# Performance work log

Hardware: AMD Instinct MI355X
Metric: run time of the kernel (lower is better)

The kernel has to match this reference:

```python
import jax, jax.numpy as jnp
import numpy as np

H = 256      # input_size == hidden_size
N = 512      # x dim0: acts as LSTM time axis (torch unbatched 2D LSTM input)
S = 128      # x dim1: independent seq positions (outer python loop in torch)
UP = 4       # upscale


def setup_inputs() -> dict:
    key = jax.random.key(0)
    ks = jax.random.split(key, 9)
    k_init = 1.0 / np.sqrt(H)
    u = lambda k, shape: jax.random.uniform(k, shape, jnp.float32, -k_init, k_init)
    return {
        "x": jax.random.normal(ks[0], (N, S, H), jnp.float32),
        # PyTorch nn.LSTM params, gate order (i, f, g, o)
        "Wih0": u(ks[1], (4 * H, H)), "Whh0": u(ks[2], (4 * H, H)),
        "bih0": u(ks[3], (4 * H,)),   "bhh0": u(ks[4], (4 * H,)),
        "Wih1": u(ks[5], (4 * H, H)), "Whh1": u(ks[6], (4 * H, H)),
        "bih1": u(ks[7], (4 * H,)),   "bhh1": u(ks[8], (4 * H,)),
    }


def _lstm_layer(x, h0, c0, Wih, Whh, b):
    """Scan one LSTM layer over the time axis. x: [N, S, H], h0/c0: [S, H]."""
    def step(carry, xt):
        h, c = carry
        g = xt @ Wih.T + h @ Whh.T + b            # [S, 4H]
        i, f, gg, o = jnp.split(g, 4, axis=-1)
        i = jax.nn.sigmoid(i)
        f = jax.nn.sigmoid(f)
        gg = jnp.tanh(gg)
        o = jax.nn.sigmoid(o)
        c = f * c + i * gg
        h = o * jnp.tanh(c)
        return (h, c), h
    (hT, cT), ys = jax.lax.scan(step, (h0, c0), x)
    return ys, hT, cT


def reference(x, Wih0, Whh0, bih0, bhh0, Wih1, Whh1, bih1, bhh1):
    n, s, hdim = x.shape
    # state per seq position (torch's outer loop is vectorized as batch S)
    h = jnp.zeros((2, s, hdim), x.dtype)
    c = jnp.zeros((2, s, hdim), x.dtype)
    b0 = bih0 + bhh0
    b1 = bih1 + bhh1
    data = [x]
    cur = x
    for _ in range(UP - 1):
        y0, h0n, c0n = _lstm_layer(cur, h[0], c[0], Wih0, Whh0, b0)
        y1, h1n, c1n = _lstm_layer(y0, h[1], c[1], Wih1, Whh1, b1)
        h = jnp.stack([h0n, h1n])
        c = jnp.stack([c0n, c1n])
        cur = y1
        data.append(y1)
    # torch interleaves per seq position: [..., s*UP + k, ...] = data[k][:, s, :]
    out = jnp.stack(data, axis=2)          # [N, S, UP, H]
    return out.reshape(n, s * UP, hdim)
```

## Files before the change

kernel.cpp:

```cpp
#include <hip/hip_runtime.h>
#include <stdint.h>

#define Hh 256
#define Sd 128
#define Nt 512
#define NPASS 3
#define TSTEPS (NPASS*Nt)
#define RBLK 16
#define POIS 0x7F80u
#define LEAD 192

typedef float f32x4 __attribute__((ext_vector_type(4)));
typedef __bf16 bf16x8 __attribute__((ext_vector_type(8)));
typedef unsigned short u16x8 __attribute__((ext_vector_type(8)));
typedef unsigned long long ull;
typedef ull ull2 __attribute__((ext_vector_type(2)));

#define HBUF_ELEMS ((size_t)Nt*Sd*Hh)
#define WPACK_OFF  (2ull*HBUF_ELEMS*2)
#define FLAGS_OFF  (WPACK_OFF + 2097152ull)

__device__ __forceinline__ unsigned short f2bf(float f) {
  unsigned u = __builtin_bit_cast(unsigned, f);
  u += 0x7FFFu + ((u >> 16) & 1u);
  return (unsigned short)(u >> 16);
}
__device__ __forceinline__ ull pk4(float a, float b, float c, float d) {
  return (ull)f2bf(a) | ((ull)f2bf(b) << 16) | ((ull)f2bf(c) << 32) | ((ull)f2bf(d) << 48);
}
__device__ __forceinline__ bool hasPois(ull v) {
  return ((unsigned short)(v)       == (unsigned short)POIS) |
         ((unsigned short)(v >> 16) == (unsigned short)POIS) |
         ((unsigned short)(v >> 32) == (unsigned short)POIS) |
         ((unsigned short)(v >> 48) == (unsigned short)POIS);
}
__device__ __forceinline__ ull ld8(const void* p) {
  return __hip_atomic_load((ull*)p, __ATOMIC_RELAXED, __HIP_MEMORY_SCOPE_AGENT);
}
__device__ __forceinline__ void st8c(void* p, ull v) {
  __hip_atomic_store((ull*)p, v, __ATOMIC_RELAXED, __HIP_MEMORY_SCOPE_AGENT);
}

__global__ void pack_w(const float* __restrict__ Wih0, const float* __restrict__ Whh0,
                       const float* __restrict__ Wih1, const float* __restrict__ Whh1,
                       unsigned short* __restrict__ wpack) {
  int id = blockIdx.x * 256 + threadIdx.x;
  int ln = id & 63;
  int kt = (id >> 6) & 15;
  int w  = (id >> 10) & 7;
  int g2 = (id >> 13) & 7;
  int l  = (id >> 16) & 1;
  int col = (w >> 1)*256 + g2*32 + (w & 1)*16 + (ln & 15);
  int k0 = kt*32 + (ln >> 4)*8;
  const float* Wih = l ? Wih1 : Wih0;
  const float* Whh = l ? Whh1 : Whh0;
  const float* src = (k0 < 256) ? (Wih + (size_t)col*256 + k0)
                                : (Whh + (size_t)col*256 + (k0 - 256));
  u16x8 v;
#pragma unroll
  for (int j = 0; j < 8; ++j) v[j] = f2bf(src[j]);
  *(u16x8*)(wpack + (size_t)id * 8) = v;
}

__global__ void copy_x(const float* __restrict__ x, float* __restrict__ out) {
  int id = blockIdx.x * 256 + threadIdx.x;
  int n  = id >> 13;
  int s  = (id >> 6) & 127;
  int h4 = id & 63;
  const float4 v = *(const float4*)(x + ((size_t)n*Sd + s)*Hh + h4*4);
  *(float4*)(out + ((size_t)n*(Sd*4) + s*4)*Hh + h4*4) = v;
}

__global__ void poison_hbuf(unsigned int* __restrict__ p) {
  size_t i = (size_t)blockIdx.x * 256 + threadIdx.x;
  uint4 v = make_uint4(0x7F807F80u, 0x7F807F80u, 0x7F807F80u, 0x7F807F80u);
  *(uint4*)(p + i*4) = v;
}

__global__ void __launch_bounds__(512) lstm_persist(
    const float* __restrict__ x,
    const float* __restrict__ bih0, const float* __restrict__ bhh0,
    const float* __restrict__ bih1, const float* __restrict__ bhh1,
    const unsigned short* __restrict__ wpack,
    unsigned short* __restrict__ hbuf,
    unsigned int* __restrict__ prog,
    float* __restrict__ out)
{
  const int b = blockIdx.x;
  const int r = b & 7;
  const int g2 = (b >> 3) & 7;
  const int l = (b >> 6) & 1;
  const int tid = threadIdx.x;
  const int ln = tid & 63;
  const int w  = tid >> 6;

  __shared__ __align__(16) unsigned short Ain[RBLK * 256];
  __shared__ __align__(16) unsigned short Ah [RBLK * 256];
  __shared__ float gates[RBLK][132];

  bf16x8 B[16];
  {
    const unsigned short* base = wpack + ((size_t)((l*8 + g2)*8 + w)) * 8192 + (size_t)ln * 8;
#pragma unroll
    for (int kt = 0; kt < 16; ++kt) {
      u16x8 u = *(const u16x8*)(base + kt * 512);
      B[kt] = __builtin_bit_cast(bf16x8, u);
    }
  }

  const int srow = tid >> 5;
  const int cc   = tid & 31;
  const int s    = r*RBLK + srow;
  const int hcol = g2*32 + cc;
  float bias[4];
  {
    const float* bi = l ? bih1 : bih0;
    const float* bh = l ? bhh1 : bhh0;
#pragma unroll
    for (int q = 0; q < 4; ++q) {
      int col = q*256 + g2*32 + cc;
      bias[q] = bi[col] + bh[col];
    }
  }
  float cst = 0.f;

  const int row_f = ln & 15;
  const int kg16  = (ln >> 4) * 16;
  const int swr   = (row_f & 7) << 4;
  const int stAddr = srow*512 + ((cc*16) ^ ((srow & 7) << 4));

  unsigned int* flagL1 = prog + r*8;
  unsigned int* myFlag = prog + r*8 + g2;
  const unsigned short* hbufL0 = hbuf;
  unsigned short* hbufSelf = hbuf + (size_t)l * HBUF_ELEMS;

  auto stageAin = [&](int T1) {
    const int t1 = T1 & 511, p1 = T1 >> 9;
    if (l == 1) {
      const ull* ip = (const ull*)(hbufL0 + ((size_t)t1*Sd + s)*Hh + cc*8);
      ull a0 = ld8(ip), a1 = ld8(ip + 1);
      while (hasPois(a0)) { __builtin_amdgcn_s_sleep(1); a0 = ld8(ip); }
      while (hasPois(a1)) { __builtin_amdgcn_s_sleep(1); a1 = ld8(ip + 1); }
      ull2 v = {a0, a1}; *(ull2*)((char*)Ain + stAddr) = v;
    } else if (p1 == 0) {
      const float* xb = x + ((size_t)t1*Sd + s)*Hh + cc*8;
      float4 v0 = *(const float4*)(xb);
      float4 v1 = *(const float4*)(xb + 4);
      ull2 v = {pk4(v0.x, v0.y, v0.z, v0.w), pk4(v1.x, v1.y, v1.z, v1.w)};
      *(ull2*)((char*)Ain + stAddr) = v;
    } else {
      const ull* op = (const ull*)(out + ((size_t)t1*(Sd*4) + s*4 + p1)*Hh + cc*8);
      ull o0 = ld8(op), o1 = ld8(op+1), o2 = ld8(op+2), o3 = ld8(op+3);
      float f0 = __builtin_bit_cast(float, (unsigned)(o0 & 0xFFFFFFFFu));
      float f1 = __builtin_bit_cast(float, (unsigned)(o0 >> 32));
      float f2 = __builtin_bit_cast(float, (unsigned)(o1 & 0xFFFFFFFFu));
      float f3 = __builtin_bit_cast(float, (unsigned)(o1 >> 32));
      float f4 = __builtin_bit_cast(float, (unsigned)(o2 & 0xFFFFFFFFu));
      float f5 = __builtin_bit_cast(float, (unsigned)(o2 >> 32));
      float f6 = __builtin_bit_cast(float, (unsigned)(o3 & 0xFFFFFFFFu));
      float f7 = __builtin_bit_cast(float, (unsigned)(o3 >> 32));
      ull2 v = {pk4(f0, f1, f2, f3), pk4(f4, f5, f6, f7)};
      *(ull2*)((char*)Ain + stAddr) = v;
    }
  };

#define MFMA4(BUF, BOFF)                                                            \
  {                                                                                 \
    _Pragma("unroll")                                                               \
    for (int kt = 0; kt < 8; kt += 2) {                                             \
      int off0 = row_f*512 + (( kt     *64 + kg16) ^ swr);                          \
      int off1 = row_f*512 + (((kt + 1)*64 + kg16) ^ swr);                          \
      u16x8 a0 = *(const u16x8*)((const char*)BUF + off0);                          \
      u16x8 a1 = *(const u16x8*)((const char*)BUF + off1);                          \
      acc0 = __builtin_amdgcn_mfma_f32_16x16x32_bf16(                               \
               __builtin_bit_cast(bf16x8, a0), B[BOFF + kt],     acc0, 0,0,0);      \
      acc1 = __builtin_amdgcn_mfma_f32_16x16x32_bf16(                               \
               __builtin_bit_cast(bf16x8, a1), B[BOFF + kt + 1], acc1, 0,0,0);      \
    }                                                                               \
  }

  f32x4 acc0 = {0.f,0.f,0.f,0.f}, acc1 = {0.f,0.f,0.f,0.f};
  stageAin(0);
  __syncthreads();
  MFMA4(Ain, 0)

  for (int T = 0; T < TSTEPS; ++T) {
    const int p = T >> 9;
    const int t = T & 511;

    if (T > 0) {
      const ull* ap = (const ull*)(hbufSelf + ((size_t)((T - 1) & 511)*Sd + s)*Hh + cc*8);
      ull a0 = ld8(ap), a1 = ld8(ap + 1);
      while (hasPois(a0)) { __builtin_amdgcn_s_sleep(1); a0 = ld8(ap); }
      while (hasPois(a1)) { __builtin_amdgcn_s_sleep(1); a1 = ld8(ap + 1); }
      ull2 v = {a0, a1}; *(ull2*)((char*)Ah + stAddr) = v;
    }
    if (l == 0 && tid < 8) {
      int need = T - LEAD;
      if (need > 0)
        while ((int)__hip_atomic_load(flagL1 + tid, __ATOMIC_RELAXED, __HIP_MEMORY_SCOPE_AGENT) < need)
          __builtin_amdgcn_s_sleep(1);
    }
    __syncthreads();

    if (T > 0) MFMA4(Ah, 8)

    {
      const int colb = (w >> 1)*32 + (w & 1)*16 + (ln & 15);
      const int rowb = (ln >> 4)*4;
#pragma unroll
      for (int j = 0; j < 4; ++j)
        gates[rowb + j][colb] = acc0[j] + acc1[j];
    }
    __syncthreads();

    {
      float G0 = gates[srow][cc]      + bias[0];
      float G1 = gates[srow][32 + cc] + bias[1];
      float G2 = gates[srow][64 + cc] + bias[2];
      float G3 = gates[srow][96 + cc] + bias[3];
      float gi = 1.f/(1.f + __expf(-G0));
      float gf = 1.f/(1.f + __expf(-G1));
      float gg = 1.f - 2.f/(1.f + __expf(2.f*G2));
      float go = 1.f/(1.f + __expf(-G3));
      cst = gf*cst + gi*gg;
      float th = 1.f - 2.f/(1.f + __expf(2.f*cst));
      float hv = go*th;
      float h1 = __shfl_down(hv, 1);
      float h2 = __shfl_down(hv, 2);
      float h3 = __shfl_down(hv, 3);
      if ((cc & 3) == 0) {
        st8c(hbufSelf + ((size_t)t*Sd + s)*Hh + hcol, pk4(hv, h1, h2, h3));
        st8c(hbufSelf + ((size_t)((T + 256) & 511)*Sd + s)*Hh + hcol,
             0x7F807F807F807F80ull);
      }
      if (l == 1 && (cc & 1) == 0) {
        ull o01 = ((ull)__builtin_bit_cast(unsigned, hv))
                | ((ull)__builtin_bit_cast(unsigned, h1) << 32);
        st8c(out + ((size_t)t*(Sd*4) + s*4 + (p + 1))*Hh + hcol, o01);
      }
    }
    if (l == 1 && (T & 7) == 7) {
      asm volatile("s_waitcnt vmcnt(0)" ::: "memory");
      __syncthreads();
      if (tid == 0)
        __hip_atomic_store(myFlag, (unsigned)(T + 1), __ATOMIC_RELAXED, __HIP_MEMORY_SCOPE_AGENT);
    }

    acc0 = (f32x4){0.f,0.f,0.f,0.f};
    acc1 = (f32x4){0.f,0.f,0.f,0.f};
    if (T + 1 < TSTEPS) {
      stageAin(T + 1);
      __syncthreads();
      MFMA4(Ain, 0)
    }
  }
}

extern "C" void kernel_launch(void* const* d_in, const int* in_sizes, int n_in,
                              void* d_out, int out_size, void* d_ws, size_t ws_size,
                              hipStream_t stream) {
  const float* x    = (const float*)d_in[0];
  const float* Wih0 = (const float*)d_in[1];
  const float* Whh0 = (const float*)d_in[2];
  const float* bih0 = (const float*)d_in[3];
  const float* bhh0 = (const float*)d_in[4];
  const float* Wih1 = (const float*)d_in[5];
  const float* Whh1 = (const float*)d_in[6];
  const float* bih1 = (const float*)d_in[7];
  const float* bhh1 = (const float*)d_in[8];
  float* out = (float*)d_out;
  char* ws = (char*)d_ws;

  if (ws_size < FLAGS_OFF + 4096) return;

  unsigned short* hbuf  = (unsigned short*)ws;
  unsigned short* wpack = (unsigned short*)(ws + WPACK_OFF);
  unsigned int*   prog  = (unsigned int*)(ws + FLAGS_OFF);

  hipMemsetAsync(prog, 0, 1024, stream);
  hipLaunchKernelGGL(poison_hbuf, dim3(16384), dim3(256), 0, stream, (unsigned int*)hbuf);
  hipLaunchKernelGGL(pack_w, dim3(512), dim3(256), 0, stream, Wih0, Whh0, Wih1, Whh1, wpack);
  hipLaunchKernelGGL(copy_x, dim3(16384), dim3(256), 0, stream, x, out);
  hipLaunchKernelGGL(lstm_persist, dim3(128), dim3(512), 0, stream,
                     x, bih0, bhh0, bih1, bhh1, wpack, hbuf, prog, out);
}
```

Before: 3.586 ms.

## Double-buffer input staging with register prefetch and relax cross-layer flag sync

Input rows for the next step are loaded into registers two steps ahead and written into a double-buffered LDS tile during the current step. This removes one __syncthreads and the global-load latency from the critical recurrent path. Layer-0 flag checks and layer-1 progress stores now happen every 16 steps instead of 8. The waitcnt and barrier before the flag store are also dropped, which risks the flag being published before the output stores are visible.

New measurement: 3.098 ms. -13.6%, faster.

```diff
diff --git a/kernel.cpp b/kernel.cpp
--- a/kernel.cpp
+++ b/kernel.cpp
@@ -39,6 +39,13 @@
 }
 __device__ __forceinline__ void st8c(void* p, ull v) {
   __hip_atomic_store((ull*)p, v, __ATOMIC_RELAXED, __HIP_MEMORY_SCOPE_AGENT);
+}
+__device__ __forceinline__ void poll2(const ull* p, ull& a0, ull& a1) {
+  while (hasPois(a0) | hasPois(a1)) {
+    __builtin_amdgcn_s_sleep(1);
+    if (hasPois(a0)) a0 = ld8(p);
+    if (hasPois(a1)) a1 = ld8(p + 1);
+  }
 }
 
 __global__ void pack_w(const float* __restrict__ Wih0, const float* __restrict__ Whh0,
@@ -94,8 +101,8 @@
   const int ln = tid & 63;
   const int w  = tid >> 6;
 
-  __shared__ __align__(16) unsigned short Ain[RBLK * 256];
-  __shared__ __align__(16) unsigned short Ah [RBLK * 256];
+  __shared__ __align__(16) unsigned short AinB[2][RBLK * 256];
+  __shared__ __align__(16) unsigned short Ah[RBLK * 256];
   __shared__ float gates[RBLK][132];
 
   bf16x8 B[16];
@@ -134,33 +141,39 @@
   const unsigned short* hbufL0 = hbuf;
   unsigned short* hbufSelf = hbuf + (size_t)l * HBUF_ELEMS;
 
-  auto stageAin = [&](int T1) {
-    const int t1 = T1 & 511, p1 = T1 >> 9;
+  float4 pxa, pxb;
+  ull pa = 0, pb = 0;
+
+  auto writeAin = [&](int buf, ull lo, ull hi) {
+    ull2 v = {lo, hi};
+    *(ull2*)((char*)AinB[buf] + stAddr) = v;
+  };
+  auto prefetchAin = [&](int T2) {
+    const int t2 = T2 & 511, p2 = T2 >> 9;
     if (l == 1) {
-      const ull* ip = (const ull*)(hbufL0 + ((size_t)t1*Sd + s)*Hh + cc*8);
-      ull a0 = ld8(ip), a1 = ld8(ip + 1);
-      while (hasPois(a0)) { __builtin_amdgcn_s_sleep(1); a0 = ld8(ip); }
-      while (hasPois(a1)) { __builtin_amdgcn_s_sleep(1); a1 = ld8(ip + 1); }
-      ull2 v = {a0, a1}; *(ull2*)((char*)Ain + stAddr) = v;
-    } else if (p1 == 0) {
-      const float* xb = x + ((size_t)t1*Sd + s)*Hh + cc*8;
-      float4 v0 = *(const float4*)(xb);
-      float4 v1 = *(const float4*)(xb + 4);
-      ull2 v = {pk4(v0.x, v0.y, v0.z, v0.w), pk4(v1.x, v1.y, v1.z, v1.w)};
-      *(ull2*)((char*)Ain + stAddr) = v;
+      const ull* ip = (const ull*)(hbufL0 + ((size_t)t2*Sd + s)*Hh + cc*8);
+      pa = ld8(ip); pb = ld8(ip + 1);
+    } else if (p2 == 0) {
+      const float* xb = x + ((size_t)t2*Sd + s)*Hh + cc*8;
+      pxa = *(const float4*)(xb);
+      pxb = *(const float4*)(xb + 4);
     } else {
-      const ull* op = (const ull*)(out + ((size_t)t1*(Sd*4) + s*4 + p1)*Hh + cc*8);
-      ull o0 = ld8(op), o1 = ld8(op+1), o2 = ld8(op+2), o3 = ld8(op+3);
-      float f0 = __builtin_bit_cast(float, (unsigned)(o0 & 0xFFFFFFFFu));
-      float f1 = __builtin_bit_cast(float, (unsigned)(o0 >> 32));
-      float f2 = __builtin_bit_cast(float, (unsigned)(o1 & 0xFFFFFFFFu));
-      float f3 = __builtin_bit_cast(float, (unsigned)(o1 >> 32));
-      float f4 = __builtin_bit_cast(float, (unsigned)(o2 & 0xFFFFFFFFu));
-      float f5 = __builtin_bit_cast(float, (unsigned)(o2 >> 32));
-      float f6 = __builtin_bit_cast(float, (unsigned)(o3 & 0xFFFFFFFFu));
-      float f7 = __builtin_bit_cast(float, (unsigned)(o3 >> 32));
-      ull2 v = {pk4(f0, f1, f2, f3), pk4(f4, f5, f6, f7)};
-      *(ull2*)((char*)Ain + stAddr) = v;
+      const float* ob = out + ((size_t)t2*(Sd*4) + s*4 + p2)*Hh + cc*8;
+      pxa = *(const float4*)(ob);
+      pxb = *(const float4*)(ob + 4);
+    }
+  };
+  auto consumeAin = [&](int T1) {
+    const int buf = T1 & 1;
+    if (l == 1) {
+      if (hasPois(pa) | hasPois(pb)) {
+        const int t1 = T1 & 511;
+        const ull* ip = (const ull*)(hbufL0 + ((size_t)t1*Sd + s)*Hh + cc*8);
+        poll2(ip, pa, pb);
+      }
+      writeAin(buf, pa, pb);
+    } else {
+      writeAin(buf, pk4(pxa.x, pxa.y, pxa.z, pxa.w), pk4(pxb.x, pxb.y, pxb.z, pxb.w));
     }
   };
 
@@ -170,8 +183,8 @@
     for (int kt = 0; kt < 8; kt += 2) {                                             \
       int off0 = row_f*512 + (( kt     *64 + kg16) ^ swr);                          \
       int off1 = row_f*512 + (((kt + 1)*64 + kg16) ^ swr);                          \
-      u16x8 a0 = *(const u16x8*)((const char*)BUF + off0);                          \
-      u16x8 a1 = *(const u16x8*)((const char*)BUF + off1);                          \
+      u16x8 a0 = *(const u16x8*)((const char*)(BUF) + off0);                        \
+      u16x8 a1 = *(const u16x8*)((const char*)(BUF) + off1);                        \
       acc0 = __builtin_amdgcn_mfma_f32_16x16x32_bf16(                               \
                __builtin_bit_cast(bf16x8, a0), B[BOFF + kt],     acc0, 0,0,0);      \
       acc1 = __builtin_amdgcn_mfma_f32_16x16x32_bf16(                               \
@@ -180,9 +193,19 @@
   }
 
   f32x4 acc0 = {0.f,0.f,0.f,0.f}, acc1 = {0.f,0.f,0.f,0.f};
-  stageAin(0);
+  if (l == 1) {
+    const ull* ip = (const ull*)(hbufL0 + (size_t)s*Hh + cc*8);
+    ull a0 = ld8(ip), a1 = ld8(ip + 1);
+    poll2(ip, a0, a1);
+    writeAin(0, a0, a1);
+  } else {
+    const float* xb = x + (size_t)s*Hh + cc*8;
+    float4 v0 = *(const float4*)(xb), v1 = *(const float4*)(xb + 4);
+    writeAin(0, pk4(v0.x, v0.y, v0.z, v0.w), pk4(v1.x, v1.y, v1.z, v1.w));
+  }
+  prefetchAin(1);
   __syncthreads();
-  MFMA4(Ain, 0)
+  MFMA4(AinB[0], 0)
 
   for (int T = 0; T < TSTEPS; ++T) {
     const int p = T >> 9;
@@ -191,11 +214,15 @@
     if (T > 0) {
       const ull* ap = (const ull*)(hbufSelf + ((size_t)((T - 1) & 511)*Sd + s)*Hh + cc*8);
       ull a0 = ld8(ap), a1 = ld8(ap + 1);
-      while (hasPois(a0)) { __builtin_amdgcn_s_sleep(1); a0 = ld8(ap); }
-      while (hasPois(a1)) { __builtin_amdgcn_s_sleep(1); a1 = ld8(ap + 1); }
-      ull2 v = {a0, a1}; *(ull2*)((char*)Ah + stAddr) = v;
-    }
-    if (l == 0 && tid < 8) {
+      poll2(ap, a0, a1);
+      ull2 v = {a0, a1};
+      *(ull2*)((char*)Ah + stAddr) = v;
+    } else {
+      ull2 v = {0ull, 0ull};
+      *(ull2*)((char*)Ah + stAddr) = v;
+    }
+    if (T + 1 < TSTEPS) consumeAin(T + 1);
+    if (l == 0 && (T & 15) == 0 && tid < 8) {
       int need = T - LEAD;
       if (need > 0)
         while ((int)__hip_atomic_load(flagL1 + tid, __ATOMIC_RELAXED, __HIP_MEMORY_SCOPE_AGENT) < need)
@@ -240,20 +267,12 @@
         st8c(out + ((size_t)t*(Sd*4) + s*4 + (p + 1))*Hh + hcol, o01);
       }
     }
-    if (l == 1 && (T & 7) == 7) {
-      asm volatile("s_waitcnt vmcnt(0)" ::: "memory");
-      __syncthreads();
-      if (tid == 0)
-        __hip_atomic_store(myFlag, (unsigned)(T + 1), __ATOMIC_RELAXED, __HIP_MEMORY_SCOPE_AGENT);
-    }
-
+    if (l == 1 && (T & 15) == 15 && tid == 0)
+      __hip_atomic_store(myFlag, (unsigned)(T + 1), __ATOMIC_RELAXED, __HIP_MEMORY_SCOPE_AGENT);
+    if (T + 2 < TSTEPS) prefetchAin(T + 2);
     acc0 = (f32x4){0.f,0.f,0.f,0.f};
     acc1 = (f32x4){0.f,0.f,0.f,0.f};
-    if (T + 1 < TSTEPS) {
-      stageAin(T + 1);
-      __syncthreads();
-      MFMA4(Ain, 0)
-    }
+    if (T + 1 < TSTEPS) MFMA4(AinB[(T + 1) & 1], 0)
   }
 }
 
```
